# Kernel optimization log

Hardware: AMD Instinct MI355X
Metric: run time of the kernel (lower is better)

The kernel has to match this reference:

```python
import jax, jax.numpy as jnp
import numpy as np
import math

EPS_LN = 1e-5
TARGET_ACTIVITY = 0.1
THETA = 2.0 ** 16

B, NH, T, D, N = 2, 12, 2048, 768, 256


def layernorm(x):
    m = jnp.mean(x, axis=-1, keepdims=True)
    v = jnp.mean((x - m) ** 2, axis=-1, keepdims=True)
    return (x - m) / jnp.sqrt(v + EPS_LN)


def get_freqs(n):
    q = jnp.floor(jnp.arange(n, dtype=jnp.float32) / 2.0) * 2.0  # quantize by 2
    return 1.0 / (THETA ** (q / n)) / (2.0 * math.pi)


def rope(phases, v):
    ph = (phases % 1.0) * (2.0 * math.pi)
    c, s = jnp.cos(ph), jnp.sin(ph)
    even = v[..., 0::2]
    odd = v[..., 1::2]
    v_rot = jnp.stack((-odd, even), axis=-1).reshape(v.shape)  # interleaved rotate
    return v * c + v_rot * s


def setup_inputs() -> dict:
    key = jax.random.key(0)
    ks = jax.random.split(key, 5)
    std = 0.02
    return {
        "x": jax.random.normal(ks[0], (B, 1, T, D), dtype=jnp.float32),
        "encoder": jax.random.normal(ks[1], (NH, D, N), dtype=jnp.float32) * std,
        "encoder_v": jax.random.normal(ks[2], (NH, D, N), dtype=jnp.float32) * std,
        "decoder": jax.random.normal(ks[3], (NH * N, D), dtype=jnp.float32) * std,
        "scale": jnp.ones((D,), dtype=jnp.float32),
        "running_activity": jnp.ones((D,), dtype=jnp.float32) * TARGET_ACTIVITY,
    }


def reference(x, encoder, encoder_v, decoder, scale, running_activity):
    Bv, _, Tv, Dv = x.shape
    nh, _, Nv = encoder.shape

    # encode + ReLU sparsify: [B,1,T,D] @ [nh,D,N] -> [B,nh,T,N]
    x_latent = jnp.einsum('bztd,hdn->bhtn', x, encoder)
    x_sparse = jax.nn.relu(x_latent)

    # RoPE on Q=K=x_sparse
    freqs = get_freqs(Nv)  # [N]
    r_phases = jnp.arange(Tv, dtype=jnp.float32)[:, None] * freqs[None, :]  # [T,N]
    QR = rope(r_phases, x_sparse)
    KR = rope(r_phases, x_sparse)

    # non-softmax causal attention, strictly lower-triangular (diag=-1)
    scores = jnp.einsum('bhtn,bhsn->bhts', QR, KR)
    mask = jnp.tril(jnp.ones((Tv, Tv), dtype=scores.dtype), k=-1)
    scores = scores * mask
    yKV = jnp.einsum('bhts,bsd->bhtd', scores, x[:, 0])  # V = x

    yKV = layernorm(yKV)
    y_sparse = jax.nn.relu(jnp.einsum('bhtd,hdn->bhtn', yKV, encoder_v))
    xy_sparse = x_sparse * y_sparse  # [B,nh,T,N]; dropout=0 (eval)

    # [B,nh,T,N] -> [B,1,T,nh*N] @ [nh*N,D]
    flat = jnp.transpose(xy_sparse, (0, 2, 1, 3)).reshape(Bv, 1, Tv, nh * Nv)
    yMLP = flat @ decoder

    y = layernorm(yMLP)
    regulation = TARGET_ACTIVITY / (running_activity + 1e-6)
    y = y * jnp.sqrt(regulation) * scale

    return layernorm(x + y), xy_sparse
```

## Files before the change

### kernel.cpp

```cpp
#include <hip/hip_runtime.h>
#include <math.h>

#define TT 2048
#define DD 768
#define NN 256
#define NHH 12
#define BB 2
#define CH 512

typedef unsigned short u16;
typedef __attribute__((ext_vector_type(8))) short bf16x8;
typedef __attribute__((ext_vector_type(8))) unsigned short u16x8;
typedef __attribute__((ext_vector_type(4))) float f32x4;

static inline int imin(int a, int b) { return a < b ? a : b; }

__device__ __forceinline__ u16 f2b(float f) {
  union { float f; unsigned u; } a; a.f = f;
  unsigned r = a.u + 0x7FFF + ((a.u >> 16) & 1);
  return (u16)(r >> 16);
}
__device__ __forceinline__ float b2f(u16 h) {
  union { unsigned u; float f; } a; a.u = ((unsigned)h) << 16;
  return a.f;
}

__device__ __forceinline__ void async16(const void* g, void* l) {
  __builtin_amdgcn_global_load_lds(
      (const __attribute__((address_space(1))) unsigned*)g,
      (__attribute__((address_space(3))) unsigned*)l, 16, 0, 0);
}

#define KSWZ(row) (((row) >> 1) & 3)

__device__ __forceinline__ void stage128x32(
    const u16* __restrict__ gbase, size_t ld, u16* lds, int tid) {
  const int w = tid >> 6, l = tid & 63;
#pragma unroll
  for (int q = 0; q < 2; ++q) {
    const int row = w * 32 + q * 16 + (l >> 2);
    const int kc = ((l & 3) ^ KSWZ(row)) << 3;
    async16(gbase + (size_t)row * ld + kc, lds + (w * 32 + q * 16) * 32);
  }
}

__device__ __forceinline__ void stage64x32(
    const u16* __restrict__ gbase, size_t ld, u16* lds, int tid) {
  const int w = tid >> 6, l = tid & 63;
  const int row = w * 16 + (l >> 2);
  const int kc = ((l & 3) ^ KSWZ(row)) << 3;
  async16(gbase + (size_t)row * ld + kc, lds + w * 512);
}

__device__ __forceinline__ void mfma_step(
    const u16* As, const u16* Bs, int wr, int wc, int lane, f32x4 acc[4][4]) {
  const int m16 = lane & 15, quad = lane >> 4;
  bf16x8 a[4], b[4];
#pragma unroll
  for (int i = 0; i < 4; ++i) {
    const int row = wr * 64 + i * 16 + m16;
    a[i] = *(const bf16x8*)&As[row * 32 + ((quad ^ KSWZ(row)) << 3)];
  }
#pragma unroll
  for (int j = 0; j < 4; ++j) {
    const int row = wc * 64 + j * 16 + m16;
    b[j] = *(const bf16x8*)&Bs[row * 32 + ((quad ^ KSWZ(row)) << 3)];
  }
#pragma unroll
  for (int i = 0; i < 4; ++i)
#pragma unroll
    for (int j = 0; j < 4; ++j)
      acc[i][j] = __builtin_amdgcn_mfma_f32_16x16x32_bf16(a[i], b[j], acc[i][j], 0, 0, 0);
}

__device__ __forceinline__ void copy_out128(
    const u16* buf, u16* g, size_t ld, int tid) {
#pragma unroll
  for (int s = 0; s < 8; ++s) {
    const int off = (s * 256 + tid) * 8;
    const int row = off >> 7, col = off & 127;
    *(u16x8*)&g[(size_t)row * ld + col] = *(const u16x8*)&buf[off];
  }
}

#define GEMM_SMEM \
  __shared__ __attribute__((aligned(16))) u16 smem[32768];

#define GEMM_VARS()                                                \
  const int tid = threadIdx.x;                                     \
  const int w = tid >> 6, lane = tid & 63;                         \
  const int wr = w >> 1, wc = w & 1;                               \
  const int col16 = lane & 15, quad = lane >> 4;                   \
  f32x4 acc[4][4];                                                 \
  _Pragma("unroll") for (int i = 0; i < 4; ++i)                    \
  _Pragma("unroll") for (int j = 0; j < 4; ++j)                    \
      acc[i][j] = (f32x4){0.f, 0.f, 0.f, 0.f};

#define GEMM_PROLOGUE() GEMM_SMEM GEMM_VARS()

#define PIPELINED_K_LOOP64(ABASE, ALD, BBASE, BLD, KTOT)                    \
  {                                                                         \
    stage128x32((ABASE), (ALD), smem, tid);                                 \
    stage128x32((ABASE) + 32, (ALD), smem + 4096, tid);                     \
    stage128x32((BBASE), (BLD), smem + 8192, tid);                          \
    stage128x32((BBASE) + 32, (BLD), smem + 12288, tid);                    \
    const int np_ = (KTOT) / 64;                                            \
    for (int pp_ = 0; pp_ < np_; ++pp_) {                                   \
      u16* cb_ = (pp_ & 1) ? smem + 16384 : smem;                           \
      u16* nb_ = (pp_ & 1) ? smem : smem + 16384;                           \
      if (pp_ + 1 < np_) {                                                  \
        const int kn_ = (pp_ + 1) * 64;                                     \
        stage128x32((ABASE) + kn_, (ALD), nb_, tid);                        \
        stage128x32((ABASE) + kn_ + 32, (ALD), nb_ + 4096, tid);            \
        stage128x32((BBASE) + kn_, (BLD), nb_ + 8192, tid);                 \
        stage128x32((BBASE) + kn_ + 32, (BLD), nb_ + 12288, tid);           \
        asm volatile("s_waitcnt vmcnt(8)" ::: "memory");                    \
      } else {                                                              \
        asm volatile("s_waitcnt vmcnt(0)" ::: "memory");                    \
      }                                                                     \
      __builtin_amdgcn_s_barrier();                                         \
      __builtin_amdgcn_sched_barrier(0);                                    \
      mfma_step(cb_, cb_ + 8192, wr, wc, lane, acc);                        \
      mfma_step(cb_ + 4096, cb_ + 12288, wr, wc, lane, acc);                \
      __builtin_amdgcn_sched_barrier(0);                                    \
      __builtin_amdgcn_s_barrier();                                         \
    }                                                                       \
  }

__device__ __forceinline__ void tcvt_body(
    const float* __restrict__ ip, u16* __restrict__ op, int R, int C,
    int bx, int by, int tid, float (*tile)[33]) {
  const int c0 = bx * 32, r0 = by * 32;
  const int tx = tid & 31, ty = tid >> 5;
#pragma unroll
  for (int p = 0; p < 4; ++p)
    tile[ty + p * 8][tx] = ip[(size_t)(r0 + ty + p * 8) * C + c0 + tx];
  __syncthreads();
#pragma unroll
  for (int p = 0; p < 4; ++p)
    op[(size_t)(c0 + ty + p * 8) * R + r0 + tx] = f2b(tile[tx][ty + p * 8]);
}

__global__ __launch_bounds__(256) void k_prep(
    const float* __restrict__ x, u16* __restrict__ X16, u16* __restrict__ XT16,
    const float* __restrict__ enc, u16* __restrict__ ENCT,
    const float* __restrict__ encv, u16* __restrict__ ENCVT,
    const float* __restrict__ dec, u16* __restrict__ DECT,
    float2* __restrict__ CS) {
  __shared__ float tile[32][33];
  const int tid = threadIdx.x;
  const int bid = blockIdx.x;
  if (bid < 3072) {
    const size_t i = ((size_t)bid * 256 + tid) * 4;
    float4 v = *(const float4*)&x[i];
    u16 o[4] = {f2b(v.x), f2b(v.y), f2b(v.z), f2b(v.w)};
    *(ushort4*)&X16[i] = *(ushort4*)o;
  } else if (bid < 6144) {
    const int b = bid - 3072;
    const int bz = b / 1536, rb = b % 1536;
    tcvt_body(x + (size_t)bz * TT * DD, XT16 + (size_t)bz * DD * TT,
              TT, DD, rb % 24, rb / 24, tid, tile);
  } else if (bid < 8448) {
    const int b = bid - 6144;
    const int bz = b / 192, rb = b % 192;
    tcvt_body(enc + (size_t)bz * DD * NN, ENCT + (size_t)bz * NN * DD,
              DD, NN, rb % 8, rb / 8, tid, tile);
  } else if (bid < 10752) {
    const int b = bid - 8448;
    const int bz = b / 192, rb = b % 192;
    tcvt_body(encv + (size_t)bz * DD * NN, ENCVT + (size_t)bz * NN * DD,
              DD, NN, rb % 8, rb / 8, tid, tile);
  } else if (bid < 13056) {
    const int b = bid - 10752;
    tcvt_body(dec, DECT, NHH * NN, DD, b % 24, b / 24, tid, tile);
  } else {
    const int idx = (bid - 13056) * 256 + tid;
    const int t = idx >> 7, n2 = idx & 127;
    const float freq = exp2f((float)(2 * n2) * -0.0625f) * 0.15915494309189535f;
    const float phase = (float)t * freq;
    const float ph = (phase - floorf(phase)) * 6.283185307179586f;
    CS[idx] = make_float2(__cosf(ph), __sinf(ph));
  }
}

__global__ __launch_bounds__(256) void k_colsum(
    const u16* __restrict__ encvt, float* __restrict__ colsum) {
  const int row = blockIdx.x * 4 + (threadIdx.x >> 6);
  const int lane = threadIdx.x & 63;
  const u16* pr = encvt + (size_t)row * DD;
  float s = 0.f;
#pragma unroll
  for (int i = 0; i < 3; ++i) {
    ushort4 v = *(const ushort4*)&pr[(lane << 2) + i * 256];
    s += b2f(v.x) + b2f(v.y) + b2f(v.z) + b2f(v.w);
  }
#pragma unroll
  for (int off = 32; off; off >>= 1) s += __shfl_xor(s, off);
  if (lane == 0) colsum[row] = s;
}

__device__ __forceinline__ int swz8(int row) { return ((row >> 3) & 7) << 3; }

__global__ __launch_bounds__(256) void k1_encode(
    const u16* __restrict__ x16, const u16* __restrict__ enct,
    const float2* __restrict__ CS,
    u16* __restrict__ qr16, u16* __restrict__ qrt16) {
  const int h = blockIdx.z;
  const int m0 = blockIdx.x * 128, n0 = blockIdx.y * 128;
  GEMM_PROLOGUE();
  PIPELINED_K_LOOP64(x16 + (size_t)m0 * DD, DD,
                     enct + ((size_t)h * NN + n0) * DD, DD, DD);
  __syncthreads();
#pragma unroll
  for (int i = 0; i < 4; ++i)
#pragma unroll
    for (int j = 0; j < 4; ++j) {
      const int n = n0 + wc * 64 + j * 16 + col16;
      float rv[4], pv[4];
#pragma unroll
      for (int r = 0; r < 4; ++r) rv[r] = fmaxf(acc[i][j][r], 0.f);
#pragma unroll
      for (int r = 0; r < 4; ++r) pv[r] = __shfl_xor(rv[r], 1);
#pragma unroll
      for (int r = 0; r < 4; ++r) {
        const int lrow = wr * 64 + i * 16 + quad * 4 + r;
        const int t = (m0 + lrow) & (TT - 1);
        const float2 cs = CS[t * 128 + (n >> 1)];
        const float o = (n & 1) ? (rv[r] * cs.x + pv[r] * cs.y)
                                : (rv[r] * cs.x - pv[r] * cs.y);
        smem[lrow * 128 + ((wc * 64 + j * 16 + col16) ^ swz8(lrow))] = f2b(o);
      }
    }
  __syncthreads();
  const int bq = m0 >> 11, tb = m0 & (TT - 1);
  const size_t sl = (size_t)(bq * NHH + h);
  u16* qg = qr16 + (sl * TT + tb) * NN + n0;
#pragma unroll
  for (int s = 0; s < 8; ++s) {
    const int off = (s * 256 + tid) * 8;
    const int row = off >> 7, col = off & 127;
    *(u16x8*)&qg[(size_t)row * NN + col] =
        *(const u16x8*)&smem[row * 128 + (col ^ swz8(row))];
  }
#pragma unroll
  for (int s = 0; s < 8; ++s) {
    const int off = (s * 256 + tid) * 8;
    const int nr = off >> 7, tc = off & 127;
    const int sw = swz8(tc);
    u16 vals[8];
#pragma unroll
    for (int k = 0; k < 8; ++k) vals[k] = smem[(tc + k) * 128 + (nr ^ sw)];
    *(u16x8*)&qrt16[(sl * NN + n0 + nr) * TT + tb + tc] = *(u16x8*)vals;
  }
}

__global__ __launch_bounds__(256) void kSB(
    const u16* __restrict__ qr16, const u16* __restrict__ xt16,
    const u16* __restrict__ qrt16, u16* __restrict__ sb,
    u16* __restrict__ h16, int nB, int bh0) {
  GEMM_SMEM;
  const int tid = threadIdx.x;
  const int w = tid >> 6, lane = tid & 63;
  const int col16 = lane & 15, quad = lane >> 4;
  if ((int)blockIdx.x >= nB) {
    const int rS = blockIdx.x - nB;
    const int wr = w >> 1, wc = w & 1;
    const int z = rS / 40, sub = rS % 40;
    const int bh = bh0 + z;
    const int cc = sub / 10, rr = sub % 10;
    int i = (int)((sqrtf(8.f * rr + 1.f) - 1.f) * 0.5f);
    while ((i + 1) * (i + 2) / 2 <= rr) ++i;
    while (i * (i + 1) / 2 > rr) --i;
    const int j = rr - i * (i + 1) / 2;
    const int t0 = (cc * 4 + i) * 128;
    const int s0 = cc * CH + j * 128;
    const u16* q = qr16 + (size_t)bh * TT * NN;
    f32x4 acc[4][4];
#pragma unroll
    for (int a = 0; a < 4; ++a)
#pragma unroll
      for (int b = 0; b < 4; ++b) acc[a][b] = (f32x4){0.f, 0.f, 0.f, 0.f};
    PIPELINED_K_LOOP64(q + (size_t)t0 * NN, NN, q + (size_t)s0 * NN, NN, NN);
    const bool diag = (i == j);
    __syncthreads();
#pragma unroll
    for (int ii = 0; ii < 4; ++ii)
#pragma unroll
      for (int jj = 0; jj < 4; ++jj) {
        const int s = s0 + wc * 64 + jj * 16 + col16;
#pragma unroll
        for (int r = 0; r < 4; ++r) {
          const int lrow = wr * 64 + ii * 16 + quad * 4 + r;
          const int t = t0 + lrow;
          float v = acc[ii][jj][r];
          if (diag && s >= t) v = 0.f;
          smem[lrow * 128 + wc * 64 + jj * 16 + col16] = f2b(v);
        }
      }
    __syncthreads();
    copy_out128(smem, sb + ((size_t)z * TT + t0) * CH + j * 128, CH, tid);
  } else {
    const int r2 = blockIdx.x;
    const int z = r2 / 24, rr2 = r2 % 24;
    const int d0 = (rr2 % 12) * 64, n0 = (rr2 / 12) * 128;
    const int bh = bh0 + z, b = bh / NHH;
    u16* buf0 = smem;
    u16* buf1 = smem + 12288;
    u16* snap = smem + 24576;
    f32x4 acc[4][2];
#pragma unroll
    for (int i = 0; i < 4; ++i)
#pragma unroll
      for (int j = 0; j < 2; ++j) acc[i][j] = (f32x4){0.f, 0.f, 0.f, 0.f};
    const u16* Ab = xt16 + ((size_t)b * DD + d0) * TT;
    const u16* Bb = qrt16 + ((size_t)bh * NN + n0) * TT;
#define KB_STAGE(buf, k0)                                                   \
  {                                                                         \
    stage64x32(Ab + (k0), TT, (buf), tid);                                  \
    stage64x32(Ab + (k0) + 32, TT, (buf) + 2048, tid);                      \
    stage128x32(Bb + (k0), TT, (buf) + 4096, tid);                          \
    stage128x32(Bb + (k0) + 32, TT, (buf) + 8192, tid);                     \
  }
    for (int c = 0; c < 3; ++c) {
      const int kbase = c * CH;
      KB_STAGE(buf0, kbase);
      for (int s = 0; s < CH / 64; ++s) {
        u16* cb = (s & 1) ? buf1 : buf0;
        u16* nb = (s & 1) ? buf0 : buf1;
        if (s + 1 < CH / 64) {
          KB_STAGE(nb, kbase + (s + 1) * 64);
          asm volatile("s_waitcnt vmcnt(6)" ::: "memory");
        } else {
          asm volatile("s_waitcnt vmcnt(0)" ::: "memory");
        }
        __builtin_amdgcn_s_barrier();
        __builtin_amdgcn_sched_barrier(0);
#pragma unroll
        for (int half = 0; half < 2; ++half) {
          bf16x8 a[4], bb[2];
#pragma unroll
          for (int i = 0; i < 4; ++i) {
            const int row = i * 16 + col16;
            a[i] = *(const bf16x8*)&cb[half * 2048 + row * 32 +
                                       ((quad ^ KSWZ(row)) << 3)];
          }
#pragma unroll
          for (int j = 0; j < 2; ++j) {
            const int row = w * 32 + j * 16 + col16;
            bb[j] = *(const bf16x8*)&cb[4096 + half * 4096 + row * 32 +
                                        ((quad ^ KSWZ(row)) << 3)];
          }
#pragma unroll
          for (int i = 0; i < 4; ++i)
#pragma unroll
            for (int j = 0; j < 2; ++j)
              acc[i][j] = __builtin_amdgcn_mfma_f32_16x16x32_bf16(a[i], bb[j], acc[i][j], 0, 0, 0);
        }
        __builtin_amdgcn_sched_barrier(0);
        __builtin_amdgcn_s_barrier();
      }
#pragma unroll
      for (int i = 0; i < 4; ++i)
#pragma unroll
        for (int j = 0; j < 2; ++j)
#pragma unroll
          for (int r = 0; r < 4; ++r)
            snap[(i * 16 + quad * 4 + r) * 128 + w * 32 + j * 16 + col16] =
                f2b(acc[i][j][r]);
      __syncthreads();
      u16* hd = h16 + (size_t)(z * 3 + c) * DD * NN;
#pragma unroll
      for (int s4 = 0; s4 < 4; ++s4) {
        const int off = (s4 * 256 + tid) * 8;
        const int row = off >> 7, col = off & 127;
        *(u16x8*)&hd[(size_t)(d0 + row) * NN + n0 + col] = *(const u16x8*)&snap[off];
      }
      __syncthreads();
    }
#undef KB_STAGE
  }
}

__device__ static const int TTORD[16] = {15, 11, 7, 14, 10, 6, 13, 9,
                                         5, 3, 12, 8, 4, 2, 1, 0};

__global__ __launch_bounds__(256) void kA_attn(
    const u16* __restrict__ qr16, const u16* __restrict__ h16,
    const u16* __restrict__ sb, const u16* __restrict__ xt16,
    u16* __restrict__ ykv16, float2* __restrict__ PART, int gsTT, int bh0) {
  GEMM_SMEM;
  const int tid = threadIdx.x;
  const int w = tid >> 6, lane = tid & 63;
  const int wr = w >> 1, wc = w & 1;
  const int col16 = lane & 15, quad = lane >> 4;
  const int nwg = gridDim.x;
  const int bid = blockIdx.x;
  const int qn = nwg >> 3, r8 = nwg & 7;
  const int xcd = bid & 7, pos = bid >> 3;
  const int wg = (xcd < r8 ? xcd * (qn + 1) : r8 * (qn + 1) + (xcd - r8) * qn) + pos;
  const int z = wg / 96;
  const int tt = TTORD[(wg / 6) & 15];
  const int dblk = wg % 6;
  const int d0 = dblk * 128;
  const int bh = bh0 + z, b = bh / NHH;
  const int c = tt >> 2, it = tt & 3;
  const int t0 = tt * 128;
  f32x4 acc[4][4];
#pragma unroll
  for (int i = 0; i < 4; ++i)
#pragma unroll
    for (int j = 0; j < 4; ++j) acc[i][j] = (f32x4){0.f, 0.f, 0.f, 0.f};

  const int c4 = (c > 0) ? 4 : 0;
  const int nP = c4 + (it + 1) * 2;
  const u16* hs = h16 + ((size_t)(z * 3 + (c > 0 ? c - 1 : 0)) * DD + d0) * NN;
  const u16* qb = qr16 + ((size_t)bh * TT + t0) * NN;
  const u16* sbb = sb + ((size_t)z * TT + t0) * CH;
  const u16* xb = xt16 + ((size_t)b * DD + d0) * TT + c * CH;

#define KA_STAGE(buf, p)                                                  \
  {                                                                       \
    const u16 *pa_, *pb_; size_t la_, lb_;                                \
    if ((p) < c4) {                                                       \
      pa_ = qb + (p) * 64; la_ = NN;                                      \
      pb_ = hs + (p) * 64; lb_ = NN;                                      \
    } else {                                                              \
      const int q_ = (p) - c4;                                            \
      const int j_ = q_ >> 1, kk_ = (q_ & 1) << 6;                        \
      pa_ = sbb + j_ * 128 + kk_; la_ = CH;                               \
      pb_ = xb + j_ * 128 + kk_; lb_ = TT;                                \
    }                                                                     \
    stage128x32(pa_, la_, (buf), tid);                                    \
    stage128x32(pa_ + 32, la_, (buf) + 4096, tid);                        \
    stage128x32(pb_, lb_, (buf) + 8192, tid);                             \
    stage128x32(pb_ + 32, lb_, (buf) + 12288, tid);                       \
  }

  u16* bufA = smem;
  u16* bufB = smem + 16384;
  KA_STAGE(bufA, 0);
  for (int p = 0; p < nP; ++p) {
    u16* cb = (p & 1) ? bufB : bufA;
    u16* nb = (p & 1) ? bufA : bufB;
    if (p + 1 < nP) {
      KA_STAGE(nb, p + 1);
      asm volatile("s_waitcnt vmcnt(8)" ::: "memory");
    } else {
      asm volatile("s_waitcnt vmcnt(0)" ::: "memory");
    }
    __builtin_amdgcn_s_barrier();
    __builtin_amdgcn_sched_barrier(0);
    mfma_step(cb, cb + 8192, wr, wc, lane, acc);
    mfma_step(cb + 4096, cb + 12288, wr, wc, lane, acc);
    __builtin_amdgcn_sched_barrier(0);
    __builtin_amdgcn_s_barrier();
  }
#undef KA_STAGE

  __syncthreads();
#pragma unroll
  for (int i = 0; i < 4; ++i)
#pragma unroll
    for (int j = 0; j < 4; ++j)
#pragma unroll
      for (int r = 0; r < 4; ++r) {
        const int lrow = wr * 64 + i * 16 + quad * 4 + r;
        smem[lrow * 128 + wc * 64 + j * 16 + col16] = f2b(acc[i][j][r]);
      }
  __syncthreads();
  float2* scratch = (float2*)&smem[16384];
  u16* yg = ykv16 + ((size_t)z * TT + t0) * DD + d0;
#pragma unroll
  for (int s = 0; s < 8; ++s) {
    const int off = (s * 256 + tid) * 8;
    const int row = off >> 7, col = off & 127;
    const u16x8 v = *(const u16x8*)&smem[off];
    *(u16x8*)&yg[(size_t)row * DD + col] = v;
    float ps = 0.f, pq = 0.f;
#pragma unroll
    for (int k = 0; k < 8; ++k) {
      const float f = b2f(v[k]);
      ps += f;
      pq += f * f;
    }
    scratch[row * 17 + (tid & 15)] = make_float2(ps, pq);
  }
  __syncthreads();
  if (tid < 128) {
    const float2* pr = &scratch[tid * 17];
    float s = 0.f, q2 = 0.f;
#pragma unroll
    for (int k = 0; k < 16; ++k) { s += pr[k].x; q2 += pr[k].y; }
    PART[(size_t)dblk * gsTT + z * TT + t0 + tid] = make_float2(s, q2);
  }
}

__global__ __launch_bounds__(256) void k4_xy(
    const u16* __restrict__ ykv16, const u16* __restrict__ encvt,
    const float2* __restrict__ CS,
    u16* __restrict__ qrxy, const float2* __restrict__ PART,
    const float* __restrict__ colsum,
    float* __restrict__ out2, int gsTT, int bh0) {
  const int z = blockIdx.z;
  const int bh = bh0 + z, h = bh % NHH;
  const int t0 = blockIdx.x * 128, n0 = blockIdx.y * 128;
  GEMM_PROLOGUE();
  const u16* Ab = ykv16 + ((size_t)z * TT + t0) * DD;
  const u16* Bb = encvt + ((size_t)h * NN + n0) * DD;
  const u16* qg = qrxy + ((size_t)bh * TT + t0) * NN + n0;
  stage128x32(Ab, DD, smem, tid);
  stage128x32(Ab + 32, DD, smem + 4096, tid);
  stage128x32(Bb, DD, smem + 8192, tid);
  stage128x32(Bb + 32, DD, smem + 12288, tid);
  const int np = DD / 64;
  for (int pp = 0; pp < np; ++pp) {
    u16* cb = (pp & 1) ? smem + 16384 : smem;
    u16* nb = (pp & 1) ? smem : smem + 16384;
    if (pp + 1 < np) {
      const int kn = (pp + 1) * 64;
      stage128x32(Ab + kn, DD, nb, tid);
      stage128x32(Ab + kn + 32, DD, nb + 4096, tid);
      stage128x32(Bb + kn, DD, nb + 8192, tid);
      stage128x32(Bb + kn + 32, DD, nb + 12288, tid);
      asm volatile("s_waitcnt vmcnt(8)" ::: "memory");
    } else {
#pragma unroll
      for (int s = 0; s < 8; ++s) {
        const int row = s * 16 + w * 4 + (lane >> 4);
        const int col = (lane & 15) * 8;
        async16(qg + (size_t)row * NN + col, smem + (s * 256 + w * 64) * 8);
      }
      asm volatile("s_waitcnt vmcnt(8)" ::: "memory");
    }
    __builtin_amdgcn_s_barrier();
    __builtin_amdgcn_sched_barrier(0);
    mfma_step(cb, cb + 8192, wr, wc, lane, acc);
    mfma_step(cb + 4096, cb + 12288, wr, wc, lane, acc);
    __builtin_amdgcn_sched_barrier(0);
    __builtin_amdgcn_s_barrier();
  }
  asm volatile("s_waitcnt vmcnt(0)" ::: "memory");
  __syncthreads();
#pragma unroll
  for (int i = 0; i < 4; ++i) {
    float muv[4], rsv[4];
#pragma unroll
    for (int r = 0; r < 4; ++r) {
      const int grow = z * TT + t0 + wr * 64 + i * 16 + quad * 4 + r;
      float s_ = 0.f, q_ = 0.f;
#pragma unroll
      for (int d = 0; d < 6; ++d) {
        const float2 p2 = PART[(size_t)d * gsTT + grow];
        s_ += p2.x;
        q_ += p2.y;
      }
      const float m_ = s_ * (1.f / 768.f);
      muv[r] = m_;
      rsv[r] = rsqrtf(q_ * (1.f / 768.f) - m_ * m_ + 1e-5f);
    }
#pragma unroll
    for (int j = 0; j < 4; ++j) {
      const int lcol = wc * 64 + j * 16 + col16;
      const int n = n0 + lcol;
      const float csum = colsum[h * NN + n];
#pragma unroll
      for (int r = 0; r < 4; ++r) {
        const int lrow = wr * 64 + i * 16 + quad * 4 + r;
        const int t = t0 + lrow;
        const float ys = fmaxf(rsv[r] * acc[i][j][r] - rsv[r] * muv[r] * csum, 0.f);
        const unsigned pq =
            *(const unsigned*)&smem[lrow * 128 + (lcol & ~1)];
        const float lo = b2f((u16)pq), hi = b2f((u16)(pq >> 16));
        const float2 cs = CS[t * 128 + (n >> 1)];
        const float xs = (n & 1) ? (hi * cs.x - lo * cs.y)
                                 : (lo * cs.x + hi * cs.y);
        const float val = ys * xs;
        out2[((size_t)bh * TT + t) * NN + n] = val;
        smem[16384 + lrow * 128 + lcol] = f2b(val);
      }
    }
  }
  __syncthreads();
  copy_out128(smem + 16384, qrxy + ((size_t)bh * TT + t0) * NN + n0, NN, tid);
}

__global__ __launch_bounds__(256) void k5_mlp(
    const u16* __restrict__ xyq, const u16* __restrict__ dect,
    float* __restrict__ ymp0, float* __restrict__ ymp1) {
  GEMM_PROLOGUE();
  const int bid = blockIdx.x;
  const int wg = (bid & 7) * 48 + (bid >> 3);
  const int kh = wg / 192;
  const int r = wg % 192;
  const int m0 = (r / 6) * 128, d0 = (r % 6) * 128;
  const int b = m0 >> 11, t0 = m0 & (TT - 1);
  const int kbase = kh * 1536;
#define K5_ST(buf, p)                                                       \
  {                                                                         \
    const int k0_ = kbase + (p) * 64, hh_ = k0_ >> 8, kk_ = k0_ & 255;      \
    const u16* pa_ = xyq + ((size_t)(b * NHH + hh_) * TT + t0) * NN + kk_;  \
    const u16* pb_ = dect + (size_t)d0 * (NHH * NN) + k0_;                  \
    stage128x32(pa_, NN, (buf), tid);                                       \
    stage128x32(pa_ + 32, NN, (buf) + 4096, tid);                           \
    stage128x32(pb_, NHH * NN, (buf) + 8192, tid);                          \
    stage128x32(pb_ + 32, NHH * NN, (buf) + 12288, tid);                    \
  }
  const int NP = 1536 / 64;
  u16* bufA = smem;
  u16* bufB = smem + 16384;
  K5_ST(bufA, 0);
  for (int p = 0; p < NP; ++p) {
    u16* cb = (p & 1) ? bufB : bufA;
    u16* nb = (p & 1) ? bufA : bufB;
    if (p + 1 < NP) {
      K5_ST(nb, p + 1);
      asm volatile("s_waitcnt vmcnt(8)" ::: "memory");
    } else {
      asm volatile("s_waitcnt vmcnt(0)" ::: "memory");
    }
    __builtin_amdgcn_s_barrier();
    __builtin_amdgcn_sched_barrier(0);
    mfma_step(cb, cb + 8192, wr, wc, lane, acc);
    mfma_step(cb + 4096, cb + 12288, wr, wc, lane, acc);
    __builtin_amdgcn_sched_barrier(0);
    __builtin_amdgcn_s_barrier();
  }
#undef K5_ST
  float* ymlp = kh ? ymp1 : ymp0;
#pragma unroll
  for (int i = 0; i < 4; ++i)
#pragma unroll
    for (int j = 0; j < 4; ++j) {
      const int d = d0 + wc * 64 + j * 16 + col16;
#pragma unroll
      for (int r4 = 0; r4 < 4; ++r4) {
        const int mm = m0 + wr * 64 + i * 16 + quad * 4 + r4;
        ymlp[(size_t)mm * DD + d] = acc[i][j][r4];
      }
    }
}

__global__ __launch_bounds__(256) void k6_final(
    const float* __restrict__ ym0, const float* __restrict__ ym1,
    const float* __restrict__ x,
    const float* __restrict__ scale, const float* __restrict__ ra,
    float* __restrict__ out1) {
  const int row = blockIdx.x;
  const int tid = threadIdx.x;
  const int wid = tid >> 6, lane = tid & 63;
  __shared__ float red[8];
  float v[3];
  float sum = 0.f, sq = 0.f;
#pragma unroll
  for (int j = 0; j < 3; ++j) {
    const size_t idx = (size_t)row * DD + tid + j * 256;
    v[j] = ym0[idx] + ym1[idx];
    sum += v[j]; sq += v[j] * v[j];
  }
#pragma unroll
  for (int off = 32; off; off >>= 1) { sum += __shfl_xor(sum, off); sq += __shfl_xor(sq, off); }
  if (lane == 0) { red[wid] = sum; red[4 + wid] = sq; }
  __syncthreads();
  sum = red[0] + red[1] + red[2] + red[3];
  sq = red[4] + red[5] + red[6] + red[7];
  const float m1 = sum * (1.f / 768.f);
  const float r1 = rsqrtf(sq * (1.f / 768.f) - m1 * m1 + 1e-5f);
  float z[3];
  float sum2 = 0.f, sq2 = 0.f;
#pragma unroll
  for (int j = 0; j < 3; ++j) {
    const int d = tid + j * 256;
    float y = (v[j] - m1) * r1 * sqrtf(0.1f / (ra[d] + 1e-6f)) * scale[d];
    z[j] = x[(size_t)row * DD + d] + y;
    sum2 += z[j]; sq2 += z[j] * z[j];
  }
  __syncthreads();
#pragma unroll
  for (int off = 32; off; off >>= 1) { sum2 += __shfl_xor(sum2, off); sq2 += __shfl_xor(sq2, off); }
  if (lane == 0) { red[wid] = sum2; red[4 + wid] = sq2; }
  __syncthreads();
  sum2 = red[0] + red[1] + red[2] + red[3];
  sq2 = red[4] + red[5] + red[6] + red[7];
  const float m2 = sum2 * (1.f / 768.f);
  const float r2 = rsqrtf(sq2 * (1.f / 768.f) - m2 * m2 + 1e-5f);
#pragma unroll
  for (int j = 0; j < 3; ++j)
    out1[(size_t)row * DD + tid + j * 256] = (z[j] - m2) * r2;
}

extern "C" void kernel_launch(void* const* d_in, const int* in_sizes, int n_in,
                              void* d_out, int out_size, void* d_ws, size_t ws_size,
                              hipStream_t stream) {
  const float* x = (const float*)d_in[0];
  const float* enc = (const float*)d_in[1];
  const float* encv = (const float*)d_in[2];
  const float* dec = (const float*)d_in[3];
  const float* scale = (const float*)d_in[4];
  const float* ra = (const float*)d_in[5];
  float* out1 = (float*)d_out;
  float* out2 = out1 + (size_t)BB * TT * DD;
  float* ym0 = out1;

  const int NS = BB * NHH;
  unsigned char* p = (unsigned char*)d_ws;
  u16* X16 = (u16*)p;    p += (size_t)BB * TT * DD * 2;
  u16* XT16 = (u16*)p;   p += (size_t)BB * DD * TT * 2;
  u16* ENCT = (u16*)p;   p += (size_t)NHH * NN * DD * 2;
  u16* ENCVT = (u16*)p;  p += (size_t)NHH * NN * DD * 2;
  u16* DECT = (u16*)p;   p += (size_t)DD * NHH * NN * 2;
  u16* QR16 = (u16*)p;   p += (size_t)NS * TT * NN * 2;
  u16* QRT16 = (u16*)p;  p += (size_t)NS * NN * TT * 2;
  float* COLSUM = (float*)p; p += (size_t)NHH * NN * 4;
  float2* CS = (float2*)p;   p += (size_t)TT * (NN / 2) * sizeof(float2);
  float* YM1 = (float*)p;    p += (size_t)BB * TT * DD * 4;
  const size_t SLICE_B = (size_t)TT * CH * 2 + 3 * (size_t)DD * NN * 2 +
                         (size_t)TT * DD * 2 + (size_t)TT * 48;
  size_t fixed = (size_t)(p - (unsigned char*)d_ws);
  size_t rem = (ws_size > fixed) ? ws_size - fixed : 0;
  int GSmax = (int)(rem / SLICE_B);
  if (GSmax < 1) GSmax = 1;
  if (GSmax > NS) GSmax = NS;
  const int ngrp = (NS + GSmax - 1) / GSmax;
  const int GS = (NS + ngrp - 1) / ngrp;
  u16* SB = (u16*)p;     p += (size_t)GS * TT * CH * 2;
  u16* H16 = (u16*)p;    p += (size_t)GS * 3 * DD * NN * 2;
  u16* YKV16 = (u16*)p;  p += (size_t)GS * TT * DD * 2;
  float2* PART = (float2*)p; p += (size_t)GS * TT * 6 * sizeof(float2);
  const int gsTT = GS * TT;

  k_prep<<<dim3(14080), 256, 0, stream>>>(
      x, X16, XT16, enc, ENCT, encv, ENCVT, dec, DECT, CS);
  k_colsum<<<dim3(NHH * NN / 4), 256, 0, stream>>>(ENCVT, COLSUM);

  k1_encode<<<dim3(BB * TT / 128, NN / 128, NHH), 256, 0, stream>>>(
      X16, ENCT, CS, QR16, QRT16);

  for (int bh0 = 0; bh0 < NS; bh0 += GS) {
    const int gs = imin(GS, NS - bh0);
    kSB<<<dim3(64 * gs), 256, 0, stream>>>(
        QR16, XT16, QRT16, SB, H16, 24 * gs, bh0);
    kA_attn<<<dim3(96 * gs), 256, 0, stream>>>(
        QR16, H16, SB, XT16, YKV16, PART, gsTT, bh0);
    k4_xy<<<dim3(TT / 128, NN / 128, gs), 256, 0, stream>>>(
        YKV16, ENCVT, CS, QR16, PART, COLSUM, out2, gsTT, bh0);
  }

  k5_mlp<<<dim3(384), 256, 0, stream>>>(QR16, DECT, ym0, YM1);
  k6_final<<<dim3(BB * TT), 256, 0, stream>>>(ym0, YM1, x, scale, ra, out1);
}
```

Before: 346.5 us.

## Enlarge kSB H-tile to 128x128, fuse colsum into prep, vectorize final layernorm

The H-computation blocks in kSB now compute 128x128 tiles (d by n) instead of 64x128. They reuse the shared mfma_step and copy_out128 helpers, halving the block count and increasing operand reuse per block. The separate k_colsum kernel is removed: colsum is accumulated with atomics inside the encoder_v transpose blocks of k_prep, after a memset. The final layernorm kernel now handles one row per wavefront using float4 loads, which removes the shared-memory reductions and barriers. The changes trade fewer, larger blocks for less parallelism, and replace a kernel launch with atomics plus a memset.

New measurement: 332.4 us. 4.1% less time.

```diff
diff --git a/kernel.cpp b/kernel.cpp
--- a/kernel.cpp
+++ b/kernel.cpp
@@ -42,14 +42,6 @@
     const int kc = ((l & 3) ^ KSWZ(row)) << 3;
     async16(gbase + (size_t)row * ld + kc, lds + (w * 32 + q * 16) * 32);
   }
-}
-
-__device__ __forceinline__ void stage64x32(
-    const u16* __restrict__ gbase, size_t ld, u16* lds, int tid) {
-  const int w = tid >> 6, l = tid & 63;
-  const int row = w * 16 + (l >> 2);
-  const int kc = ((l & 3) ^ KSWZ(row)) << 3;
-  async16(gbase + (size_t)row * ld + kc, lds + w * 512);
 }
 
 __device__ __forceinline__ void mfma_step(
@@ -146,7 +138,7 @@
     const float* __restrict__ enc, u16* __restrict__ ENCT,
     const float* __restrict__ encv, u16* __restrict__ ENCVT,
     const float* __restrict__ dec, u16* __restrict__ DECT,
-    float2* __restrict__ CS) {
+    float2* __restrict__ CS, float* __restrict__ colsum) {
   __shared__ float tile[32][33];
   const int tid = threadIdx.x;
   const int bid = blockIdx.x;
@@ -170,6 +162,12 @@
     const int bz = b / 192, rb = b % 192;
     tcvt_body(encv + (size_t)bz * DD * NN, ENCVT + (size_t)bz * NN * DD,
               DD, NN, rb % 8, rb / 8, tid, tile);
+    if (tid < 32) {
+      float s = 0.f;
+#pragma unroll
+      for (int d = 0; d < 32; ++d) s += b2f(f2b(tile[d][tid]));
+      atomicAdd(&colsum[bz * NN + (rb % 8) * 32 + tid], s);
+    }
   } else if (bid < 13056) {
     const int b = bid - 10752;
     tcvt_body(dec, DECT, NHH * NN, DD, b % 24, b / 24, tid, tile);
@@ -183,22 +181,6 @@
   }
 }
 
-__global__ __launch_bounds__(256) void k_colsum(
-    const u16* __restrict__ encvt, float* __restrict__ colsum) {
-  const int row = blockIdx.x * 4 + (threadIdx.x >> 6);
-  const int lane = threadIdx.x & 63;
-  const u16* pr = encvt + (size_t)row * DD;
-  float s = 0.f;
-#pragma unroll
-  for (int i = 0; i < 3; ++i) {
-    ushort4 v = *(const ushort4*)&pr[(lane << 2) + i * 256];
-    s += b2f(v.x) + b2f(v.y) + b2f(v.z) + b2f(v.w);
-  }
-#pragma unroll
-  for (int off = 32; off; off >>= 1) s += __shfl_xor(s, off);
-  if (lane == 0) colsum[row] = s;
-}
-
 __device__ __forceinline__ int swz8(int row) { return ((row >> 3) & 7) << 3; }
 
 __global__ __launch_bounds__(256) void k1_encode(
@@ -261,10 +243,10 @@
   GEMM_SMEM;
   const int tid = threadIdx.x;
   const int w = tid >> 6, lane = tid & 63;
+  const int wr = w >> 1, wc = w & 1;
   const int col16 = lane & 15, quad = lane >> 4;
   if ((int)blockIdx.x >= nB) {
     const int rS = blockIdx.x - nB;
-    const int wr = w >> 1, wc = w & 1;
     const int z = rS / 40, sub = rS % 40;
     const int bh = bh0 + z;
     const int cc = sub / 10, rr = sub % 10;
@@ -301,83 +283,56 @@
     copy_out128(smem, sb + ((size_t)z * TT + t0) * CH + j * 128, CH, tid);
   } else {
     const int r2 = blockIdx.x;
-    const int z = r2 / 24, rr2 = r2 % 24;
-    const int d0 = (rr2 % 12) * 64, n0 = (rr2 / 12) * 128;
+    const int z = r2 / 12, rr2 = r2 % 12;
+    const int d0 = (rr2 % 6) * 128, n0 = (rr2 / 6) * 128;
     const int bh = bh0 + z, b = bh / NHH;
-    u16* buf0 = smem;
-    u16* buf1 = smem + 12288;
-    u16* snap = smem + 24576;
-    f32x4 acc[4][2];
-#pragma unroll
-    for (int i = 0; i < 4; ++i)
-#pragma unroll
-      for (int j = 0; j < 2; ++j) acc[i][j] = (f32x4){0.f, 0.f, 0.f, 0.f};
+    f32x4 acc[4][4];
+#pragma unroll
+    for (int a = 0; a < 4; ++a)
+#pragma unroll
+      for (int b2 = 0; b2 < 4; ++b2) acc[a][b2] = (f32x4){0.f, 0.f, 0.f, 0.f};
     const u16* Ab = xt16 + ((size_t)b * DD + d0) * TT;
     const u16* Bb = qrt16 + ((size_t)bh * NN + n0) * TT;
-#define KB_STAGE(buf, k0)                                                   \
-  {                                                                         \
-    stage64x32(Ab + (k0), TT, (buf), tid);                                  \
-    stage64x32(Ab + (k0) + 32, TT, (buf) + 2048, tid);                      \
-    stage128x32(Bb + (k0), TT, (buf) + 4096, tid);                          \
-    stage128x32(Bb + (k0) + 32, TT, (buf) + 8192, tid);                     \
-  }
     for (int c = 0; c < 3; ++c) {
       const int kbase = c * CH;
-      KB_STAGE(buf0, kbase);
+      stage128x32(Ab + kbase, TT, smem, tid);
+      stage128x32(Ab + kbase + 32, TT, smem + 4096, tid);
+      stage128x32(Bb + kbase, TT, smem + 8192, tid);
+      stage128x32(Bb + kbase + 32, TT, smem + 12288, tid);
       for (int s = 0; s < CH / 64; ++s) {
-        u16* cb = (s & 1) ? buf1 : buf0;
-        u16* nb = (s & 1) ? buf0 : buf1;
+        u16* cb = (s & 1) ? smem + 16384 : smem;
+        u16* nb = (s & 1) ? smem : smem + 16384;
         if (s + 1 < CH / 64) {
-          KB_STAGE(nb, kbase + (s + 1) * 64);
-          asm volatile("s_waitcnt vmcnt(6)" ::: "memory");
+          const int kn = kbase + (s + 1) * 64;
+          stage128x32(Ab + kn, TT, nb, tid);
+          stage128x32(Ab + kn + 32, TT, nb + 4096, tid);
+          stage128x32(Bb + kn, TT, nb + 8192, tid);
+          stage128x32(Bb + kn + 32, TT, nb + 12288, tid);
+          asm volatile("s_waitcnt vmcnt(8)" ::: "memory");
         } else {
           asm volatile("s_waitcnt vmcnt(0)" ::: "memory");
         }
         __builtin_amdgcn_s_barrier();
         __builtin_amdgcn_sched_barrier(0);
-#pragma unroll
-        for (int half = 0; half < 2; ++half) {
-          bf16x8 a[4], bb[2];
-#pragma unroll
-          for (int i = 0; i < 4; ++i) {
-            const int row = i * 16 + col16;
-            a[i] = *(const bf16x8*)&cb[half * 2048 + row * 32 +
-                                       ((quad ^ KSWZ(row)) << 3)];
-          }
-#pragma unroll
-          for (int j = 0; j < 2; ++j) {
-            const int row = w * 32 + j * 16 + col16;
-            bb[j] = *(const bf16x8*)&cb[4096 + half * 4096 + row * 32 +
-                                        ((quad ^ KSWZ(row)) << 3)];
-          }
-#pragma unroll
-          for (int i = 0; i < 4; ++i)
-#pragma unroll
-            for (int j = 0; j < 2; ++j)
-              acc[i][j] = __builtin_amdgcn_mfma_f32_16x16x32_bf16(a[i], bb[j], acc[i][j], 0, 0, 0);
-        }
+        mfma_step(cb, cb + 8192, wr, wc, lane, acc);
+        mfma_step(cb + 4096, cb + 12288, wr, wc, lane, acc);
         __builtin_amdgcn_sched_barrier(0);
         __builtin_amdgcn_s_barrier();
       }
+      __syncthreads();
 #pragma unroll
       for (int i = 0; i < 4; ++i)
 #pragma unroll
-        for (int j = 0; j < 2; ++j)
-#pragma unroll
-          for (int r = 0; r < 4; ++r)
-            snap[(i * 16 + quad * 4 + r) * 128 + w * 32 + j * 16 + col16] =
-                f2b(acc[i][j][r]);
+        for (int j = 0; j < 4; ++j)
+#pragma unroll
+          for (int r = 0; r < 4; ++r) {
+            const int lrow = wr * 64 + i * 16 + quad * 4 + r;
+            smem[lrow * 128 + wc * 64 + j * 16 + col16] = f2b(acc[i][j][r]);
+          }
       __syncthreads();
-      u16* hd = h16 + (size_t)(z * 3 + c) * DD * NN;
-#pragma unroll
-      for (int s4 = 0; s4 < 4; ++s4) {
-        const int off = (s4 * 256 + tid) * 8;
-        const int row = off >> 7, col = off & 127;
-        *(u16x8*)&hd[(size_t)(d0 + row) * NN + n0 + col] = *(const u16x8*)&snap[off];
-      }
+      copy_out128(smem, h16 + ((size_t)(z * 3 + c) * DD + d0) * NN + n0, NN, tid);
       __syncthreads();
     }
-#undef KB_STAGE
   }
 }
 
@@ -645,47 +600,55 @@
     const float* __restrict__ x,
     const float* __restrict__ scale, const float* __restrict__ ra,
     float* __restrict__ out1) {
-  const int row = blockIdx.x;
-  const int tid = threadIdx.x;
-  const int wid = tid >> 6, lane = tid & 63;
-  __shared__ float red[8];
-  float v[3];
+  const int row = blockIdx.x * 4 + (threadIdx.x >> 6);
+  const int lane = threadIdx.x & 63;
+  const size_t base = (size_t)row * DD;
+  float4 v[3];
   float sum = 0.f, sq = 0.f;
 #pragma unroll
-  for (int j = 0; j < 3; ++j) {
-    const size_t idx = (size_t)row * DD + tid + j * 256;
-    v[j] = ym0[idx] + ym1[idx];
-    sum += v[j]; sq += v[j] * v[j];
+  for (int k = 0; k < 3; ++k) {
+    const size_t idx = base + k * 256 + lane * 4;
+    const float4 a = *(const float4*)&ym0[idx];
+    const float4 b = *(const float4*)&ym1[idx];
+    v[k] = make_float4(a.x + b.x, a.y + b.y, a.z + b.z, a.w + b.w);
+    sum += v[k].x + v[k].y + v[k].z + v[k].w;
+    sq += v[k].x * v[k].x + v[k].y * v[k].y + v[k].z * v[k].z + v[k].w * v[k].w;
   }
 #pragma unroll
   for (int off = 32; off; off >>= 1) { sum += __shfl_xor(sum, off); sq += __shfl_xor(sq, off); }
-  if (lane == 0) { red[wid] = sum; red[4 + wid] = sq; }
-  __syncthreads();
-  sum = red[0] + red[1] + red[2] + red[3];
-  sq = red[4] + red[5] + red[6] + red[7];
   const float m1 = sum * (1.f / 768.f);
   const float r1 = rsqrtf(sq * (1.f / 768.f) - m1 * m1 + 1e-5f);
-  float z[3];
+  float4 z[3];
   float sum2 = 0.f, sq2 = 0.f;
 #pragma unroll
-  for (int j = 0; j < 3; ++j) {
-    const int d = tid + j * 256;
-    float y = (v[j] - m1) * r1 * sqrtf(0.1f / (ra[d] + 1e-6f)) * scale[d];
-    z[j] = x[(size_t)row * DD + d] + y;
-    sum2 += z[j]; sq2 += z[j] * z[j];
-  }
-  __syncthreads();
+  for (int k = 0; k < 3; ++k) {
+    const int d = k * 256 + lane * 4;
+    const float4 sc = *(const float4*)&scale[d];
+    const float4 rv = *(const float4*)&ra[d];
+    const float4 xv = *(const float4*)&x[base + d];
+    float4 zz;
+    zz.x = xv.x + (v[k].x - m1) * r1 * sqrtf(0.1f / (rv.x + 1e-6f)) * sc.x;
+    zz.y = xv.y + (v[k].y - m1) * r1 * sqrtf(0.1f / (rv.y + 1e-6f)) * sc.y;
+    zz.z = xv.z + (v[k].z - m1) * r1 * sqrtf(0.1f / (rv.z + 1e-6f)) * sc.z;
+    zz.w = xv.w + (v[k].w - m1) * r1 * sqrtf(0.1f / (rv.w + 1e-6f)) * sc.w;
+    z[k] = zz;
+    sum2 += zz.x + zz.y + zz.z + zz.w;
+    sq2 += zz.x * zz.x + zz.y * zz.y + zz.z * zz.z + zz.w * zz.w;
+  }
 #pragma unroll
   for (int off = 32; off; off >>= 1) { sum2 += __shfl_xor(sum2, off); sq2 += __shfl_xor(sq2, off); }
-  if (lane == 0) { red[wid] = sum2; red[4 + wid] = sq2; }
-  __syncthreads();
-  sum2 = red[0] + red[1] + red[2] + red[3];
-  sq2 = red[4] + red[5] + red[6] + red[7];
   const float m2 = sum2 * (1.f / 768.f);
   const float r2 = rsqrtf(sq2 * (1.f / 768.f) - m2 * m2 + 1e-5f);
 #pragma unroll
-  for (int j = 0; j < 3; ++j)
-    out1[(size_t)row * DD + tid + j * 256] = (z[j] - m2) * r2;
+  for (int k = 0; k < 3; ++k) {
+    const int d = k * 256 + lane * 4;
+    float4 o;
+    o.x = (z[k].x - m2) * r2;
+    o.y = (z[k].y - m2) * r2;
+    o.z = (z[k].z - m2) * r2;
+    o.w = (z[k].w - m2) * r2;
+    *(float4*)&out1[base + d] = o;
+  }
 }
 
 extern "C" void kernel_launch(void* const* d_in, const int* in_sizes, int n_in,
@@ -728,17 +691,17 @@
   float2* PART = (float2*)p; p += (size_t)GS * TT * 6 * sizeof(float2);
   const int gsTT = GS * TT;
 
+  hipMemsetAsync(COLSUM, 0, (size_t)NHH * NN * 4, stream);
   k_prep<<<dim3(14080), 256, 0, stream>>>(
-      x, X16, XT16, enc, ENCT, encv, ENCVT, dec, DECT, CS);
-  k_colsum<<<dim3(NHH * NN / 4), 256, 0, stream>>>(ENCVT, COLSUM);
+      x, X16, XT16, enc, ENCT, encv, ENCVT, dec, DECT, CS, COLSUM);
 
   k1_encode<<<dim3(BB * TT / 128, NN / 128, NHH), 256, 0, stream>>>(
       X16, ENCT, CS, QR16, QRT16);
 
   for (int bh0 = 0; bh0 < NS; bh0 += GS) {
     const int gs = imin(GS, NS - bh0);
-    kSB<<<dim3(64 * gs), 256, 0, stream>>>(
-        QR16, XT16, QRT16, SB, H16, 24 * gs, bh0);
+    kSB<<<dim3(52 * gs), 256, 0, stream>>>(
+        QR16, XT16, QRT16, SB, H16, 12 * gs, bh0);
     kA_attn<<<dim3(96 * gs), 256, 0, stream>>>(
         QR16, H16, SB, XT16, YKV16, PART, gsTT, bh0);
     k4_xy<<<dim3(TT / 128, NN / 128, gs), 256, 0, stream>>>(
@@ -746,5 +709,5 @@
   }
 
   k5_mlp<<<dim3(384), 256, 0, stream>>>(QR16, DECT, ym0, YM1);
-  k6_final<<<dim3(BB * TT), 256, 0, stream>>>(ym0, YM1, x, scale, ra, out1);
-}
+  k6_final<<<dim3(BB * TT / 4), 256, 0, stream>>>(ym0, YM1, x, scale, ra, out1);
+}
```
